# Performance work log

Hardware: AMD Instinct MI355X
Metric: run time of the kernel (lower is better)

The kernel has to match this reference:

```python
import jax, jax.numpy as jnp
import numpy as np

N_NODES = 100000
N_EDGES = 1250000
E_FEAT = 64
IN_CH = 128
OUT_CH = 128


def setup_inputs() -> dict:
    key = jax.random.key(0)
    k1, k2, k3, k4, k5, k6, k7 = jax.random.split(key, 7)
    edge_index = jax.random.randint(k1, (2, N_EDGES), 0, N_NODES, dtype=jnp.int64 if jax.config.jax_enable_x64 else jnp.int32)
    edge_attr = jax.random.normal(k2, (N_EDGES, E_FEAT), dtype=jnp.float32)
    node_attr = jax.random.normal(k3, (N_NODES, IN_CH), dtype=jnp.float32)
    edge_weight = jax.random.uniform(k4, (N_EDGES,), dtype=jnp.float32)
    node_weight = jax.random.uniform(k5, (N_NODES,), dtype=jnp.float32)
    # Linear(in_channels + edge_features, out_channels): weight [out, in], bias [out]
    fan_in = IN_CH + E_FEAT
    bound = 1.0 / np.sqrt(fan_in)
    W = jax.random.uniform(k6, (OUT_CH, fan_in), minval=-bound, maxval=bound, dtype=jnp.float32)
    b = jax.random.uniform(k7, (OUT_CH,), minval=-bound, maxval=bound, dtype=jnp.float32)
    return {"edge_index": edge_index, "edge_attr": edge_attr, "node_attr": node_attr,
            "edge_weight": edge_weight, "node_weight": node_weight, "W": W, "b": b}


def reference(edge_index, edge_attr, node_attr, edge_weight, node_weight, W, b):
    num_nodes = node_attr.shape[0]  # original derives from edge_index.max()+1; static here for jit
    ea = edge_attr * edge_weight[:, None]                      # [E, F] weighted edge features
    tgt = edge_index[0]                                        # [E] target node per edge
    seg_sum = jax.ops.segment_sum(ea, tgt, num_segments=num_nodes)            # [N, F]
    cnt = jax.ops.segment_sum(jnp.ones((ea.shape[0],), ea.dtype), tgt, num_segments=num_nodes)  # [N]
    edge_mean = seg_sum / jnp.maximum(cnt, 1.0)[:, None]       # scatter_mean; zero-degree -> 0
    h = jnp.concatenate([node_attr, edge_mean], axis=1)        # [N, in+F]
    out = jax.nn.relu(h @ W.T + b)                             # [N, out]
    return out * node_weight[:, None]
```

## Files before the change

kernel.cpp:

```cpp
#include <hip/hip_runtime.h>


#define EF 64
#define IN_CH 128
#define OUT_CH 128
#define K_TOT 192

__global__ __launch_bounds__(256) void degree_kernel(
    const int* __restrict__ tgt, int* __restrict__ deg, int E)
{
    const int e = blockIdx.x * blockDim.x + threadIdx.x;
    if (e < E) atomicAdd(&deg[tgt[e]], 1);
}

__global__ __launch_bounds__(256) void assign_kernel(
    const int* __restrict__ deg, int* __restrict__ cursor0,
    int* __restrict__ base, int* __restrict__ cursor, int N)
{
    const int n = blockIdx.x * blockDim.x + threadIdx.x;
    if (n < N) {
        const int b = atomicAdd(cursor0, deg[n]);
        base[n] = b;
        cursor[n] = b;
    }
}

__global__ __launch_bounds__(256) void reorder_kernel(
    const int* __restrict__ tgt, int* __restrict__ cursor,
    int* __restrict__ perm, int E)
{
    const int e = blockIdx.x * blockDim.x + threadIdx.x;
    if (e < E) {
        const int pos = atomicAdd(&cursor[tgt[e]], 1);
        perm[pos] = e;
    }
}

__global__ __launch_bounds__(256) void gather_mean_kernel(
    const float* __restrict__ edge_attr,
    const float* __restrict__ edge_weight,
    const int* __restrict__ perm,
    const int* __restrict__ base,
    const int* __restrict__ deg,
    float* __restrict__ mean,
    int N)
{
    const int n = (blockIdx.x * blockDim.x + threadIdx.x) >> 6;
    const int lane = threadIdx.x & 63;
    if (n >= N) return;

    const int s = base[n];
    const int d = deg[n];
    float acc = 0.0f;
    for (int i = 0; i < d; ++i) {
        const int e = perm[s + i];
        acc += edge_attr[(size_t)e * EF + lane] * edge_weight[e];
    }
    mean[(size_t)n * EF + lane] = acc / (float)max(d, 1);
}

#define NB 64
#define KT 64
#define HP 68

__device__ __forceinline__ int wpos(int o) {
    return ((o >> 3) << 2) + (o & 3) + ((o & 4) ? 64 : 0);
}

__global__ __launch_bounds__(256) void node_gemm_kernel(
    const float* __restrict__ node_attr,
    const float* __restrict__ mean,
    const float* __restrict__ W,
    const float* __restrict__ b,
    const float* __restrict__ node_weight,
    float* __restrict__ out,
    int N)
{
    __shared__ float W_lds[KT * OUT_CH];
    __shared__ float h_lds[KT * HP];

    const int tid   = threadIdx.x;
    const int node0 = blockIdx.x * NB;

    const int oc = tid & 15;
    const int o0 = oc * 8;
    const int n0 = (tid >> 4) * 4;

    const int s_node = tid >> 2;
    const int s_k0   = (tid & 3) * 16;
    const int w_o    = tid & 127;
    const int w_kh   = (tid >> 7) * 32;
    const int w_p    = wpos(w_o);

    float acc[4][8];
#pragma unroll
    for (int n = 0; n < 4; ++n)
#pragma unroll
        for (int j = 0; j < 8; ++j) acc[n][j] = 0.0f;

    const int gs_node = node0 + s_node;

    for (int kt = 0; kt < 3; ++kt) {
        const int k0 = kt * KT;
        __syncthreads();

        {
            const float* src = W + (size_t)w_o * K_TOT + k0 + w_kh;
#pragma unroll
            for (int i = 0; i < 32; i += 4) {
                const float4 wv = *reinterpret_cast<const float4*>(src + i);
                W_lds[(w_kh + i + 0) * OUT_CH + w_p] = wv.x;
                W_lds[(w_kh + i + 1) * OUT_CH + w_p] = wv.y;
                W_lds[(w_kh + i + 2) * OUT_CH + w_p] = wv.z;
                W_lds[(w_kh + i + 3) * OUT_CH + w_p] = wv.w;
            }
        }

        if (gs_node < N) {
            const float* src = (kt < 2)
                ? node_attr + (size_t)gs_node * IN_CH + k0 + s_k0
                : mean      + (size_t)gs_node * EF   + s_k0;
#pragma unroll
            for (int i = 0; i < 16; i += 4) {
                const float4 hv = *reinterpret_cast<const float4*>(src + i);
                h_lds[(s_k0 + i + 0) * HP + s_node] = hv.x;
                h_lds[(s_k0 + i + 1) * HP + s_node] = hv.y;
                h_lds[(s_k0 + i + 2) * HP + s_node] = hv.z;
                h_lds[(s_k0 + i + 3) * HP + s_node] = hv.w;
            }
        }
        __syncthreads();

#pragma unroll 4
        for (int k = 0; k < KT; ++k) {
            const float4 hv = *reinterpret_cast<const float4*>(&h_lds[k * HP + n0]);
            const float4 w0 = *reinterpret_cast<const float4*>(&W_lds[k * OUT_CH + oc * 4]);
            const float4 w1 = *reinterpret_cast<const float4*>(&W_lds[k * OUT_CH + 64 + oc * 4]);
            const float hh[4] = {hv.x, hv.y, hv.z, hv.w};
            const float ww[8] = {w0.x, w0.y, w0.z, w0.w, w1.x, w1.y, w1.z, w1.w};
#pragma unroll
            for (int n = 0; n < 4; ++n)
#pragma unroll
                for (int j = 0; j < 8; ++j)
                    acc[n][j] = fmaf(hh[n], ww[j], acc[n][j]);
        }
    }

    const float4 b0 = *reinterpret_cast<const float4*>(b + o0);
    const float4 b1 = *reinterpret_cast<const float4*>(b + o0 + 4);
    const float bb[8] = {b0.x, b0.y, b0.z, b0.w, b1.x, b1.y, b1.z, b1.w};

#pragma unroll
    for (int n = 0; n < 4; ++n) {
        const int gn = node0 + n0 + n;
        if (gn < N) {
            const float nw = node_weight[gn];
            float r[8];
#pragma unroll
            for (int j = 0; j < 8; ++j)
                r[j] = fmaxf(acc[n][j] + bb[j], 0.0f) * nw;
            float* dst = out + (size_t)gn * OUT_CH + o0;
            *reinterpret_cast<float4*>(dst)     = make_float4(r[0], r[1], r[2], r[3]);
            *reinterpret_cast<float4*>(dst + 4) = make_float4(r[4], r[5], r[6], r[7]);
        }
    }
}

extern "C" void kernel_launch(void* const* d_in, const int* in_sizes, int n_in,
                              void* d_out, int out_size, void* d_ws, size_t ws_size,
                              hipStream_t stream) {
    const int*   edge_index  = (const int*)d_in[0];
    const float* edge_attr   = (const float*)d_in[1];
    const float* node_attr   = (const float*)d_in[2];
    const float* edge_weight = (const float*)d_in[3];
    const float* node_weight = (const float*)d_in[4];
    const float* W           = (const float*)d_in[5];
    const float* b           = (const float*)d_in[6];
    float* out = (float*)d_out;

    const int E = in_sizes[0] / 2;
    const int N = in_sizes[2] / IN_CH;

    int*   deg     = (int*)d_ws;
    int*   cursor0 = deg + N;
    int*   base    = cursor0 + 1;
    int*   cursor  = base + N;
    int*   perm    = cursor + N;
    float* mean    = (float*)(perm + E);

    hipMemsetAsync(deg, 0, (size_t)(N + 1) * sizeof(int), stream);

    const int eb = (E + 255) / 256;
    const int nb = (N + 255) / 256;

    degree_kernel <<<eb, 256, 0, stream>>>(edge_index, deg, E);
    assign_kernel <<<nb, 256, 0, stream>>>(deg, cursor0, base, cursor, N);
    reorder_kernel<<<eb, 256, 0, stream>>>(edge_index, cursor, perm, E);

    const int gb = (N + 3) / 4;
    gather_mean_kernel<<<gb, 256, 0, stream>>>(
        edge_attr, edge_weight, perm, base, deg, mean, N);

    const int gemm_blocks = (N + NB - 1) / NB;
    node_gemm_kernel<<<gemm_blocks, 256, 0, stream>>>(
        node_attr, mean, W, b, node_weight, out, N);
}
```

Measured before the change: 824.7 us.

## Scan-based offsets, pack edge weight into CSR records, unroll gather loop

```diff
diff --git a/kernel.cpp b/kernel.cpp
--- a/kernel.cpp
+++ b/kernel.cpp
@@ -17,29 +17,52 @@
     const int* __restrict__ deg, int* __restrict__ cursor0,
     int* __restrict__ base, int* __restrict__ cursor, int N)
 {
-    const int n = blockIdx.x * blockDim.x + threadIdx.x;
-    if (n < N) {
-        const int b = atomicAdd(cursor0, deg[n]);
-        base[n] = b;
-        cursor[n] = b;
-    }
+    const int tid  = threadIdx.x;
+    const int n    = blockIdx.x * 256 + tid;
+    const int lane = tid & 63;
+    const int wv   = tid >> 6;
+
+    const int d = (n < N) ? deg[n] : 0;
+
+    int x = d;
+#pragma unroll
+    for (int off = 1; off < 64; off <<= 1) {
+        const int y = __shfl_up(x, off);
+        if (lane >= off) x += y;
+    }
+
+    __shared__ int wsum[4];
+    __shared__ int bbase;
+    if (lane == 63) wsum[wv] = x;
+    __syncthreads();
+
+    if (tid == 0) {
+        const int blockSum = wsum[0] + wsum[1] + wsum[2] + wsum[3];
+        bbase = atomicAdd(cursor0, blockSum);
+    }
+    __syncthreads();
+
+    int prev = 0;
+    for (int w = 0; w < wv; ++w) prev += wsum[w];
+
+    const int b = bbase + prev + (x - d);
+    if (n < N) { base[n] = b; cursor[n] = b; }
 }
 
 __global__ __launch_bounds__(256) void reorder_kernel(
-    const int* __restrict__ tgt, int* __restrict__ cursor,
-    int* __restrict__ perm, int E)
+    const int* __restrict__ tgt, const float* __restrict__ edge_weight,
+    int* __restrict__ cursor, int2* __restrict__ rec, int E)
 {
     const int e = blockIdx.x * blockDim.x + threadIdx.x;
     if (e < E) {
         const int pos = atomicAdd(&cursor[tgt[e]], 1);
-        perm[pos] = e;
+        rec[pos] = make_int2(e, __float_as_int(edge_weight[e]));
     }
 }
 
 __global__ __launch_bounds__(256) void gather_mean_kernel(
     const float* __restrict__ edge_attr,
-    const float* __restrict__ edge_weight,
-    const int* __restrict__ perm,
+    const int2* __restrict__ rec,
     const int* __restrict__ base,
     const int* __restrict__ deg,
     float* __restrict__ mean,
@@ -49,14 +72,32 @@
     const int lane = threadIdx.x & 63;
     if (n >= N) return;
 
-    const int s = base[n];
+    const int2* __restrict__ r = rec + base[n];
     const int d = deg[n];
-    float acc = 0.0f;
-    for (int i = 0; i < d; ++i) {
-        const int e = perm[s + i];
-        acc += edge_attr[(size_t)e * EF + lane] * edge_weight[e];
-    }
-    mean[(size_t)n * EF + lane] = acc / (float)max(d, 1);
+
+    float a0 = 0.0f, a1 = 0.0f, a2 = 0.0f, a3 = 0.0f;
+    int i = 0;
+    for (; i + 4 <= d; i += 4) {
+        const int2 r0 = r[i + 0];
+        const int2 r1 = r[i + 1];
+        const int2 r2 = r[i + 2];
+        const int2 r3 = r[i + 3];
+        const float v0 = edge_attr[(size_t)r0.x * EF + lane];
+        const float v1 = edge_attr[(size_t)r1.x * EF + lane];
+        const float v2 = edge_attr[(size_t)r2.x * EF + lane];
+        const float v3 = edge_attr[(size_t)r3.x * EF + lane];
+        a0 = fmaf(v0, __int_as_float(r0.y), a0);
+        a1 = fmaf(v1, __int_as_float(r1.y), a1);
+        a2 = fmaf(v2, __int_as_float(r2.y), a2);
+        a3 = fmaf(v3, __int_as_float(r3.y), a3);
+    }
+    for (; i < d; ++i) {
+        const int2 ri = r[i];
+        a0 = fmaf(edge_attr[(size_t)ri.x * EF + lane], __int_as_float(ri.y), a0);
+    }
+
+    const float s = (a0 + a1) + (a2 + a3);
+    mean[(size_t)n * EF + lane] = s / (float)max(d, 1);
 }
 
 #define NB 64
@@ -185,8 +226,8 @@
     int*   cursor0 = deg + N;
     int*   base    = cursor0 + 1;
     int*   cursor  = base + N;
-    int*   perm    = cursor + N;
-    float* mean    = (float*)(perm + E);
+    int2*  rec     = (int2*)(cursor + N);
+    float* mean    = (float*)(rec + E);
 
     hipMemsetAsync(deg, 0, (size_t)(N + 1) * sizeof(int), stream);
 
@@ -195,11 +236,11 @@
 
     degree_kernel <<<eb, 256, 0, stream>>>(edge_index, deg, E);
     assign_kernel <<<nb, 256, 0, stream>>>(deg, cursor0, base, cursor, N);
-    reorder_kernel<<<eb, 256, 0, stream>>>(edge_index, cursor, perm, E);
+    reorder_kernel<<<eb, 256, 0, stream>>>(edge_index, edge_weight, cursor, rec, E);
 
     const int gb = (N + 3) / 4;
     gather_mean_kernel<<<gb, 256, 0, stream>>>(
-        edge_attr, edge_weight, perm, base, deg, mean, N);
+        edge_attr, rec, base, deg, mean, N);
 
     const int gemm_blocks = (N + NB - 1) / NB;
     node_gemm_kernel<<<gemm_blocks, 256, 0, stream>>>(
```

Measured after the change: 711.0 us. -13.8%, faster.
